# Optimization experiments

Hardware: AMD Instinct MI355X
Metric: run time of the kernel (lower is better)

Reference implementation:

```python
import jax, jax.numpy as jnp
import numpy as np

RC = 5.2                                   # radial cutoff Rcr
ETA_R = np.array([16.0], dtype=np.float32)
SHF_R = (0.9 + 0.26875 * np.arange(16)).astype(np.float32)
NUM_SPECIES = 4                             # len(vocabulary)


def setup_inputs() -> dict:
    key = jax.random.key(0)
    kp, ks = jax.random.split(key)
    B, N = 64, 256
    # random positions in a 12 A box -> realistic distance matrices
    pos = jax.random.uniform(kp, (B, N, 3), jnp.float32, 0.0, 12.0)
    diff = pos[:, :, None, :] - pos[:, None, :, :]
    d = jnp.sqrt(jnp.sum(diff * diff, axis=-1) + 1e-12)
    d = d * (1.0 - jnp.eye(N, dtype=jnp.float32))  # zero self-distance
    species = jax.random.randint(ks, (B, N), 1, NUM_SPECIES + 1, jnp.int32)
    return {"distance_matrices_batch": d, "num_species_batch": species}


def reference(distance_matrices_batch, num_species_batch):
    d = distance_matrices_batch                      # [B, N, N]
    eta = jnp.asarray(ETA_R)
    shf = jnp.asarray(SHF_R)
    # cartesian product of (EtaR, ShfR), P = len(EtaR)*len(ShfR)
    eta_p = jnp.repeat(eta, shf.shape[0])            # [P]
    shf_p = jnp.tile(shf, eta.shape[0])              # [P]

    mask = (d < RC) & (d != 0.0)                     # [B, N, N]
    fc = 0.5 * jnp.cos(jnp.pi * d / RC) + 0.5        # ANAKIN cutoff fn
    # Gaussian radial terms, masked to the cutoff neighborhood
    terms = jnp.exp(-eta_p * (d[..., None] - shf_p) ** 2) * fc[..., None]  # [B,N,N,P]
    terms = jnp.where(mask[..., None], terms, jnp.zeros((), terms.dtype))

    # one-hot of neighbor species (IDs are 1-based)
    oh = jax.nn.one_hot(num_species_batch - 1, NUM_SPECIES, dtype=terms.dtype)  # [B,N,S]
    # scatter-sum over neighbors j, bucketed by species of j
    GR = jnp.einsum('bijp,bjs->bisp', terms, oh)     # [B, N, S, P]
    B, N = d.shape[0], d.shape[1]
    return GR.reshape(B, N, NUM_SPECIES * terms.shape[-1])  # [B, N, S*P]
```

## Files before the change

kernel.cpp:

```cpp
#include <hip/hip_runtime.h>
#include <hip/hip_bf16.h>
#include <stdint.h>


static __device__ __forceinline__ float bf2f(uint32_t b16) {
    union { uint32_t u; float f; } cv; cv.u = b16 << 16; return cv.f;
}

__global__ __launch_bounds__(256) void aev_kernel(
    const void* __restrict__ dmat_raw,
    const int* __restrict__ species,
    float* __restrict__ out)
{
    __shared__ int   spc[272];
    __shared__ float dsh[4][272];
    __shared__ float wsh[4][272];
    __shared__ float red[4][4][16][4];
    __shared__ int   flag32;

    const int tid  = threadIdx.x;
    const int w    = tid >> 6;
    const int lane = tid & 63;
    const int row  = (int)blockIdx.x * 4 + w;
    const int b    = row >> 8;

    if (tid == 0) {
        const float* f = (const float*)dmat_raw;
        int ok = 1;
        #pragma unroll
        for (int k = 1; k <= 8; ++k) ok &= (f[k * 257] == 0.0f) ? 1 : 0;
        flag32 = ok;
    }
    spc[(tid >> 6) * 68 + (tid & 63)] = species[(b << 8) + tid] - 1;
    __syncthreads();

    float d[4];
    if (flag32 != 0) {
        const float4* rp = (const float4*)((const float*)dmat_raw + ((size_t)row << 8));
        float4 v = rp[lane];
        d[0] = v.x; d[1] = v.y; d[2] = v.z; d[3] = v.w;
    } else {
        const uint2* rp = (const uint2*)((const uint16_t*)dmat_raw + ((size_t)row << 8));
        uint2 u = rp[lane];
        d[0] = bf2f(u.x & 0xffffu); d[1] = bf2f(u.x >> 16);
        d[2] = bf2f(u.y & 0xffffu); d[3] = bf2f(u.y >> 16);
    }

    {
        const int base = (lane >> 4) * 68 + ((4 * lane) & 63);
        #pragma unroll
        for (int e = 0; e < 4; ++e) {
            float dd = d[e];
            bool  v  = (dd < 5.2f) && (dd != 0.0f);
            float x  = v ? dd : 2.6f;
            float fc = 0.5f * __builtin_amdgcn_cosf(x * (0.5f / 5.2f)) + 0.5f;
            dsh[w][base + e] = v ? dd : 0.0f;
            wsh[w][base + e] = v ? fc : 0.0f;
        }
    }
    __syncthreads();

    const int q = lane >> 4;
    const int p = lane & 15;
    const float shfp = 0.9f + 0.26875f * (float)p;
    float a0 = 0.0f, a1 = 0.0f, a2 = 0.0f, a3 = 0.0f;
    const int j0 = q * 68;
    for (int jj = 0; jj < 64; ++jj) {
        float dj = dsh[w][j0 + jj];
        float wj = wsh[w][j0 + jj];
        int   s  = spc[j0 + jj];
        float u  = dj - shfp;
        float t = __builtin_amdgcn_exp2f(u * u * -23.083120654223414f) * wj;
        a0 += (s == 0) ? t : 0.0f;
        a1 += (s == 1) ? t : 0.0f;
        a2 += (s == 2) ? t : 0.0f;
        a3 += (s == 3) ? t : 0.0f;
    }

    red[w][0][p][q] = a0;
    red[w][1][p][q] = a1;
    red[w][2][p][q] = a2;
    red[w][3][p][q] = a3;
    __syncthreads();

    if (lane < 16) {
        const size_t base = ((size_t)row << 6) + (size_t)lane;
        #pragma unroll
        for (int s = 0; s < 4; ++s) {
            float v = red[w][s][lane][0] + red[w][s][lane][1]
                    + red[w][s][lane][2] + red[w][s][lane][3];
            out[base + ((size_t)s << 4)] = v;
        }
    }
}

extern "C" void kernel_launch(void* const* d_in, const int* in_sizes, int n_in,
                              void* d_out, int out_size, void* d_ws, size_t ws_size,
                              hipStream_t stream) {
    const void* dmat   = d_in[0];
    const int* species = (const int*)d_in[1];
    float* o           = (float*)d_out;
    const int B = in_sizes[1] >> 8;
    aev_kernel<<<dim3(B * 64), 256, 0, stream>>>(dmat, species, o);
}
```

Baseline: 90.07 us.

## Compact in-cutoff neighbors by species via ballot before radial accumulation

Each block now handles 16 rows and uses wave ballots plus mbcnt to stream-compact only the neighbors inside the cutoff into shared memory, grouped by species. Each thread (row, shift) then loops only over the valid neighbors of each species, with no per-element species selects. Most of the exp work on out-of-cutoff pairs is skipped, at the cost of ballot and popcount overhead, a data-dependent loop length, and fewer blocks. The runtime fp32/bf16 input detection is dropped and the kernel assumes fp32 input.

Measured after the change: 101.1 us. +12.2%, slower.

```diff
diff --git a/kernel.cpp b/kernel.cpp
--- a/kernel.cpp
+++ b/kernel.cpp
@@ -1,105 +1,118 @@
 #include <hip/hip_runtime.h>
-#include <hip/hip_bf16.h>
 #include <stdint.h>
 
 
-static __device__ __forceinline__ float bf2f(uint32_t b16) {
-    union { uint32_t u; float f; } cv; cv.u = b16 << 16; return cv.f;
+static __device__ __forceinline__ int mbcnt64(uint64_t m) {
+    int lo = __builtin_amdgcn_mbcnt_lo((uint32_t)m, 0u);
+    return __builtin_amdgcn_mbcnt_hi((uint32_t)(m >> 32), lo);
 }
 
 __global__ __launch_bounds__(256) void aev_kernel(
-    const void* __restrict__ dmat_raw,
+    const float* __restrict__ dmat,
     const int* __restrict__ species,
     float* __restrict__ out)
 {
-    __shared__ int   spc[272];
-    __shared__ float dsh[4][272];
-    __shared__ float wsh[4][272];
-    __shared__ float red[4][4][16][4];
-    __shared__ int   flag32;
+    __shared__ int    rbase[16][5];
+    __shared__ float2 comp[16][258];
 
     const int tid  = threadIdx.x;
     const int w    = tid >> 6;
     const int lane = tid & 63;
-    const int row  = (int)blockIdx.x * 4 + w;
-    const int b    = row >> 8;
+    const int blk  = (int)blockIdx.x;
+    const int b    = blk >> 4;
 
-    if (tid == 0) {
-        const float* f = (const float*)dmat_raw;
-        int ok = 1;
-        #pragma unroll
-        for (int k = 1; k <= 8; ++k) ok &= (f[k * 257] == 0.0f) ? 1 : 0;
-        flag32 = ok;
-    }
-    spc[(tid >> 6) * 68 + (tid & 63)] = species[(b << 8) + tid] - 1;
-    __syncthreads();
+    const int4 s4 = ((const int4*)(species + (b << 8)))[lane];
+    const int sv[4] = {s4.x - 1, s4.y - 1, s4.z - 1, s4.w - 1};
 
-    float d[4];
-    if (flag32 != 0) {
-        const float4* rp = (const float4*)((const float*)dmat_raw + ((size_t)row << 8));
-        float4 v = rp[lane];
-        d[0] = v.x; d[1] = v.y; d[2] = v.z; d[3] = v.w;
-    } else {
-        const uint2* rp = (const uint2*)((const uint16_t*)dmat_raw + ((size_t)row << 8));
-        uint2 u = rp[lane];
-        d[0] = bf2f(u.x & 0xffffu); d[1] = bf2f(u.x >> 16);
-        d[2] = bf2f(u.y & 0xffffu); d[3] = bf2f(u.y >> 16);
-    }
+    for (int rr = 0; rr < 4; ++rr) {
+        const int r = (w << 2) + rr;
+        const float4* rp = (const float4*)(dmat + ((size_t)(blk * 16 + r) << 8));
+        float4 q4 = rp[lane];
+        float d[4] = {q4.x, q4.y, q4.z, q4.w};
 
-    {
-        const int base = (lane >> 4) * 68 + ((4 * lane) & 63);
+        float dc[4], fw[4]; bool valid[4];
         #pragma unroll
         for (int e = 0; e < 4; ++e) {
-            float dd = d[e];
-            bool  v  = (dd < 5.2f) && (dd != 0.0f);
-            float x  = v ? dd : 2.6f;
+            bool v = (d[e] < 5.2f) && (d[e] != 0.0f);
+            float x = v ? d[e] : 2.6f;
             float fc = 0.5f * __builtin_amdgcn_cosf(x * (0.5f / 5.2f)) + 0.5f;
-            dsh[w][base + e] = v ? dd : 0.0f;
-            wsh[w][base + e] = v ? fc : 0.0f;
+            valid[e] = v; dc[e] = x; fw[e] = fc;
+        }
+
+        uint64_t bal[4][4];
+        #pragma unroll
+        for (int e = 0; e < 4; ++e) {
+            uint64_t bv = __ballot(valid[e]);
+            uint64_t b0 = __ballot((sv[e] & 1) != 0);
+            uint64_t b1 = __ballot((sv[e] & 2) != 0);
+            bal[e][0] = bv & ~b0 & ~b1;
+            bal[e][1] = bv &  b0 & ~b1;
+            bal[e][2] = bv & ~b0 &  b1;
+            bal[e][3] = bv &  b0 &  b1;
+        }
+
+        int sb[5];
+        sb[0] = 0;
+        #pragma unroll
+        for (int s = 0; s < 4; ++s)
+            sb[s + 1] = sb[s] + __popcll(bal[0][s]) + __popcll(bal[1][s])
+                               + __popcll(bal[2][s]) + __popcll(bal[3][s]);
+
+        int run[4];
+        #pragma unroll
+        for (int s = 0; s < 4; ++s) run[s] = sb[s];
+
+        #pragma unroll
+        for (int e = 0; e < 4; ++e) {
+            const int s = sv[e];
+            uint64_t m = bal[e][0];
+            m = (s == 1) ? bal[e][1] : m;
+            m = (s == 2) ? bal[e][2] : m;
+            m = (s == 3) ? bal[e][3] : m;
+            int base = run[0];
+            base = (s == 1) ? run[1] : base;
+            base = (s == 2) ? run[2] : base;
+            base = (s == 3) ? run[3] : base;
+            int slot = base + mbcnt64(m);
+            slot = (slot < 257) ? slot : 257;
+            if (valid[e]) comp[r][slot] = make_float2(dc[e], fw[e]);
+            #pragma unroll
+            for (int s2 = 0; s2 < 4; ++s2) run[s2] += __popcll(bal[e][s2]);
+        }
+
+        if (lane == 0) {
+            #pragma unroll
+            for (int s = 0; s <= 4; ++s) rbase[r][s] = sb[s];
         }
     }
     __syncthreads();
 
-    const int q = lane >> 4;
-    const int p = lane & 15;
+    const int ti = tid >> 4;
+    const int p  = tid & 15;
     const float shfp = 0.9f + 0.26875f * (float)p;
-    float a0 = 0.0f, a1 = 0.0f, a2 = 0.0f, a3 = 0.0f;
-    const int j0 = q * 68;
-    for (int jj = 0; jj < 64; ++jj) {
-        float dj = dsh[w][j0 + jj];
-        float wj = wsh[w][j0 + jj];
-        int   s  = spc[j0 + jj];
-        float u  = dj - shfp;
-        float t = __builtin_amdgcn_exp2f(u * u * -23.083120654223414f) * wj;
-        a0 += (s == 0) ? t : 0.0f;
-        a1 += (s == 1) ? t : 0.0f;
-        a2 += (s == 2) ? t : 0.0f;
-        a3 += (s == 3) ? t : 0.0f;
-    }
+    const size_t ob = (((size_t)blk * 16 + (size_t)ti) << 6) + (size_t)p;
 
-    red[w][0][p][q] = a0;
-    red[w][1][p][q] = a1;
-    red[w][2][p][q] = a2;
-    red[w][3][p][q] = a3;
-    __syncthreads();
-
-    if (lane < 16) {
-        const size_t base = ((size_t)row << 6) + (size_t)lane;
-        #pragma unroll
-        for (int s = 0; s < 4; ++s) {
-            float v = red[w][s][lane][0] + red[w][s][lane][1]
-                    + red[w][s][lane][2] + red[w][s][lane][3];
-            out[base + ((size_t)s << 4)] = v;
+    #pragma unroll
+    for (int s = 0; s < 4; ++s) {
+        const int beg = rbase[ti][s];
+        const int end = rbase[ti][s + 1];
+        float acc = 0.0f;
+        for (int k = beg; k < end; ++k) {
+            float2 dw = comp[ti][k];
+            float u = dw.x - shfp;
+            float t = __builtin_amdgcn_exp2f(u * u * -23.083120654223414f);
+            acc = __builtin_fmaf(t, dw.y, acc);
         }
+        out[ob + ((size_t)s << 4)] = acc;
     }
 }
 
 extern "C" void kernel_launch(void* const* d_in, const int* in_sizes, int n_in,
                               void* d_out, int out_size, void* d_ws, size_t ws_size,
                               hipStream_t stream) {
-    const void* dmat   = d_in[0];
+    const float* dmat  = (const float*)d_in[0];
     const int* species = (const int*)d_in[1];
     float* o           = (float*)d_out;
     const int B = in_sizes[1] >> 8;
-    aev_kernel<<<dim3(B * 64), 256, 0, stream>>>(dmat, species, o);
+    aev_kernel<<<dim3(B * 16), 256, 0, stream>>>(dmat, species, o);
 }
```
